# Kernel optimization log

Measured on AMD Instinct MI355X. Metric: run time of the kernel, lower is better.

The kernel has to match this reference:

```python
import jax, jax.numpy as jnp
import numpy as np

TAU = 0.8
N, D = 4096, 512

def _proj(x, W, b):
    # nn.Linear then ELU (torch Linear: x @ W.T + b)
    return jax.nn.elu(x @ W.T + b)

def setup_inputs() -> dict:
    key = jax.random.key(0)
    k1, k2, k3, k4, k5 = jax.random.split(key, 5)
    v1 = jax.random.normal(k1, (N, D), dtype=jnp.float32)
    v2 = jax.random.normal(k2, (N, D), dtype=jnp.float32)
    pos = jax.random.uniform(k3, (N, N), dtype=jnp.float32)
    neg = jax.random.uniform(k4, (N, N), dtype=jnp.float32)
    W = jax.random.normal(k5, (D, D), dtype=jnp.float32) * (1.414 / np.sqrt(D))
    b = jnp.zeros((D,), dtype=jnp.float32)
    return {"v1_embs": v1, "v2_embs": v2, "pos": pos, "neg": neg, "W_proj": W, "b_proj": b}

def reference(v1_embs, v2_embs, pos, neg, W_proj, b_proj):
    z1 = _proj(v1_embs, W_proj, b_proj)
    z2 = _proj(v2_embs, W_proj, b_proj)
    # cosine-similarity style: dot / (|z1||z2|) / tau, then exp
    n1 = jnp.linalg.norm(z1, axis=-1, keepdims=True)  # [N,1]
    n2 = jnp.linalg.norm(z2, axis=-1, keepdims=True)  # [N,1]
    dots = z1 @ z2.T                                   # [N,N]
    sim = jnp.exp(dots / (n1 * n2.T) / TAU)
    sim_pos = sim * pos
    sim_neg = sim * neg
    ratio = sim_pos.sum() / (sim_pos + sim_neg).sum()
    return -jnp.log(ratio)
```

## Files before the change

### kernel.cpp

```cpp
#include <hip/hip_runtime.h>
#include <hip/hip_bf16.h>
#include <math.h>

#define NROWS 4096
#define DDIM  512
#define INV_TAU 1.25f
#define SROW 132

typedef __attribute__((ext_vector_type(8))) short short8;
typedef __attribute__((ext_vector_type(4))) float f32x4;

__device__ inline void gload_lds16(const void* g, void* l) {
  __builtin_amdgcn_global_load_lds(
      (const __attribute__((address_space(1))) void*)g,
      (__attribute__((address_space(3))) void*)l, 16, 0, 0);
}

__device__ inline unsigned short f2bf(float f) {
  __hip_bfloat16 h = __float2bfloat16(f);
  return __builtin_bit_cast(unsigned short, h);
}
__device__ inline float bf2f(unsigned short u) {
  return __bfloat162float(__builtin_bit_cast(__hip_bfloat16, u));
}

__global__ void convert_kernel(const float* __restrict__ v1,
                               const float* __restrict__ v2,
                               const float* __restrict__ W,
                               unsigned short* __restrict__ v1b,
                               unsigned short* __restrict__ v2b,
                               unsigned short* __restrict__ Wb,
                               float* __restrict__ nsq1,
                               float* __restrict__ nsq2) {
  int idx = blockIdx.x * blockDim.x + threadIdx.x;
  if (idx < NROWS) { nsq1[idx] = 0.f; nsq2[idx] = 0.f; }
  const int TOTV = (NROWS * DDIM) / 4;
  const int TOTW = (DDIM * DDIM) / 4;
  const int total = 2 * TOTV + TOTW;
  const int stride = gridDim.x * blockDim.x;
  for (int i = idx; i < total; i += stride) {
    const float4* src; unsigned short* dst; int j;
    if (i < TOTV)            { src = (const float4*)v1; dst = v1b; j = i; }
    else if (i < 2 * TOTV)   { src = (const float4*)v2; dst = v2b; j = i - TOTV; }
    else                     { src = (const float4*)W;  dst = Wb;  j = i - 2 * TOTV; }
    float4 x = src[j];
    ushort4 o;
    o.x = f2bf(x.x); o.y = f2bf(x.y); o.z = f2bf(x.z); o.w = f2bf(x.w);
    *(ushort4*)&dst[j * 4] = o;
  }
}

#define MM_CORE(Ag, Bg)                                                        \
  {                                                                            \
    for (int kt = 0; kt < DDIM; kt += 32) {                                    \
      _Pragma("unroll")                                                        \
      for (int i = 0; i < 2; ++i) {                                            \
        int off = i * 4096 + tid * 16;            \
        int row = off >> 6;                       \
        int kb  = off & 63;                                                    \
        gload_lds16((const char*)((Ag) + row * DDIM + kt) + kb,                \
                    (char*)As + i * 4096 + wid * 1024);                        \
        gload_lds16((const char*)((Bg) + row * DDIM + kt) + kb,                \
                    (char*)Bs + i * 4096 + wid * 1024);                        \
      }                                                                        \
      asm volatile("s_waitcnt vmcnt(0)" ::: "memory");                         \
      __syncthreads();                                                         \
      short8 av[4], bv[4];                                                     \
      _Pragma("unroll")                                                        \
      for (int m = 0; m < 4; ++m)                                              \
        av[m] = *(const short8*)&As[(wm * 64 + m * 16 + l15) * 32 + l4 * 8];   \
      _Pragma("unroll")                                                        \
      for (int n = 0; n < 4; ++n)                                              \
        bv[n] = *(const short8*)&Bs[(wn * 64 + n * 16 + l15) * 32 + l4 * 8];   \
      _Pragma("unroll")                                                        \
      for (int m = 0; m < 4; ++m)                                              \
        _Pragma("unroll")                                                      \
        for (int n = 0; n < 4; ++n)                                            \
          acc[m][n] = __builtin_amdgcn_mfma_f32_16x16x32_bf16(                 \
              av[m], bv[n], acc[m][n], 0, 0, 0);                               \
      __syncthreads();                                                         \
    }                                                                          \
  }

__global__ __launch_bounds__(256) void proj_kernel(
    const unsigned short* __restrict__ v1b, const unsigned short* __restrict__ v2b,
    const unsigned short* __restrict__ Wb,  const float* __restrict__ bias,
    unsigned short* __restrict__ z1b, unsigned short* __restrict__ z2b,
    float* __restrict__ nsq1, float* __restrict__ nsq2) {
  __shared__ __align__(16) unsigned short As[128 * 32];
  __shared__ __align__(16) unsigned short Bs[128 * 32];
  const int tid = threadIdx.x;
  const int wid = tid >> 6, lane = tid & 63;
  const int wm = wid >> 1, wn = wid & 1;
  const int l15 = lane & 15, l4 = lane >> 4;

  const int zsel = blockIdx.z;
  const unsigned short* Ag = (zsel ? v2b : v1b) + (size_t)blockIdx.y * 128 * DDIM;
  const unsigned short* Bg = Wb + (size_t)blockIdx.x * 128 * DDIM;
  unsigned short* Z = (zsel ? z2b : z1b);
  float* nsq = (zsel ? nsq2 : nsq1);

  f32x4 acc[4][4];
#pragma unroll
  for (int m = 0; m < 4; ++m)
#pragma unroll
    for (int n = 0; n < 4; ++n) acc[m][n] = (f32x4){0.f, 0.f, 0.f, 0.f};

  MM_CORE(Ag, Bg);

  const int rowBase = blockIdx.y * 128 + wm * 64;
  const int colBase = blockIdx.x * 128 + wn * 64;
  float bcol[4];
#pragma unroll
  for (int n = 0; n < 4; ++n) bcol[n] = bias[colBase + n * 16 + l15];
#pragma unroll
  for (int m = 0; m < 4; ++m) {
#pragma unroll
    for (int reg = 0; reg < 4; ++reg) {
      int gRow = rowBase + m * 16 + l4 * 4 + reg;
      float rs = 0.f;
#pragma unroll
      for (int n = 0; n < 4; ++n) {
        int gCol = colBase + n * 16 + l15;
        float y = acc[m][n][reg] + bcol[n];
        float zv = (y > 0.f) ? y : expm1f(y);
        unsigned short zb = f2bf(zv);
        Z[(size_t)gRow * DDIM + gCol] = zb;
        float zf = bf2f(zb);
        rs += zf * zf;
      }
      rs += __shfl_xor(rs, 1, 64);
      rs += __shfl_xor(rs, 2, 64);
      rs += __shfl_xor(rs, 4, 64);
      rs += __shfl_xor(rs, 8, 64);
      if (l15 == 0) atomicAdd(&nsq[gRow], rs);
    }
  }
}

__global__ __launch_bounds__(256) void dots_kernel(
    const unsigned short* __restrict__ z1b, const unsigned short* __restrict__ z2b,
    const float* __restrict__ nsq1, const float* __restrict__ nsq2,
    const float* __restrict__ pos, const float* __restrict__ neg,
    double* __restrict__ partials) {
  __shared__ __align__(16) char smem[32 * SROW * 4];
  unsigned short* As = (unsigned short*)smem;
  unsigned short* Bs = (unsigned short*)(smem + 8192);
  float* sCh = (float*)smem;

  const int tid = threadIdx.x;
  const int wid = tid >> 6, lane = tid & 63;
  const int wm = wid >> 1, wn = wid & 1;
  const int l15 = lane & 15, l4 = lane >> 4;

  const unsigned short* Ag = z1b + (size_t)blockIdx.y * 128 * DDIM;
  const unsigned short* Bg = z2b + (size_t)blockIdx.x * 128 * DDIM;

  f32x4 acc[4][4];
#pragma unroll
  for (int m = 0; m < 4; ++m)
#pragma unroll
    for (int n = 0; n < 4; ++n) acc[m][n] = (f32x4){0.f, 0.f, 0.f, 0.f};

  MM_CORE(Ag, Bg);

  const int blockRow = blockIdx.y * 128;
  const int blockCol = blockIdx.x * 128;
  const int rowBase = blockRow + wm * 64;
  const int colBase = blockCol + wn * 64;

  float rs2[4];
#pragma unroll
  for (int n = 0; n < 4; ++n) rs2[n] = rsqrtf(nsq2[colBase + n * 16 + l15]);

  const int lr = tid >> 3;
  const int lcBase = (tid & 7) * 16;
  const int gRowRbase = blockRow + (lr >> 4) * 64 + (lr & 15);
  const int lrW = wm * 16 + l4 * 4;
  const int lcW = wn * 64 + l15;

  float sumP = 0.f, sumT = 0.f;
#pragma unroll
  for (int m = 0; m < 4; ++m) {
    const float* pr = pos + (size_t)(gRowRbase + m * 16) * NROWS + blockCol + lcBase;
    const float* gr = neg + (size_t)(gRowRbase + m * 16) * NROWS + blockCol + lcBase;
    float4 pv[4], gv[4];
#pragma unroll
    for (int i = 0; i < 4; ++i) {
      pv[i] = *(const float4*)(pr + 4 * i);
      gv[i] = *(const float4*)(gr + 4 * i);
    }
#pragma unroll
    for (int reg = 0; reg < 4; ++reg) {
      float rs1 = rsqrtf(nsq1[rowBase + m * 16 + l4 * 4 + reg]);
#pragma unroll
      for (int n = 0; n < 4; ++n) {
        float s = __expf(acc[m][n][reg] * (rs1 * rs2[n]) * INV_TAU);
        sCh[(lrW + reg) * SROW + lcW + n * 16] = s;
      }
    }
    __syncthreads();
#pragma unroll
    for (int i = 0; i < 4; ++i) {
      float4 s4 = *(const float4*)&sCh[lr * SROW + lcBase + 4 * i];
      sumP += s4.x * pv[i].x + s4.y * pv[i].y + s4.z * pv[i].z + s4.w * pv[i].w;
      sumT += s4.x * (pv[i].x + gv[i].x) + s4.y * (pv[i].y + gv[i].y) +
              s4.z * (pv[i].z + gv[i].z) + s4.w * (pv[i].w + gv[i].w);
    }
    __syncthreads();
  }

#pragma unroll
  for (int sft = 1; sft < 64; sft <<= 1) {
    sumP += __shfl_xor(sumP, sft, 64);
    sumT += __shfl_xor(sumT, sft, 64);
  }
  __shared__ float redP[4], redT[4];
  if (lane == 0) { redP[wid] = sumP; redT[wid] = sumT; }
  __syncthreads();
  if (tid == 0) {
    double tp = (double)redP[0] + redP[1] + redP[2] + redP[3];
    double tt = (double)redT[0] + redT[1] + redT[2] + redT[3];
    int bid = blockIdx.y * gridDim.x + blockIdx.x;
    partials[2 * bid]     = tp;
    partials[2 * bid + 1] = tt;
  }
}

__global__ void finalize_kernel(const double* __restrict__ partials,
                                float* __restrict__ out) {
  __shared__ double sp[256], st[256];
  int t = threadIdx.x;
  double a = 0.0, b = 0.0;
  for (int i = t; i < 1024; i += 256) {
    a += partials[2 * i];
    b += partials[2 * i + 1];
  }
  sp[t] = a; st[t] = b;
  __syncthreads();
  for (int s = 128; s > 0; s >>= 1) {
    if (t < s) { sp[t] += sp[t + s]; st[t] += st[t + s]; }
    __syncthreads();
  }
  if (t == 0) out[0] = (float)(log(st[0]) - log(sp[0]));
}

extern "C" void kernel_launch(void* const* d_in, const int* in_sizes, int n_in,
                              void* d_out, int out_size, void* d_ws, size_t ws_size,
                              hipStream_t stream) {
  (void)in_sizes; (void)n_in; (void)out_size; (void)ws_size;
  const float* v1   = (const float*)d_in[0];
  const float* v2   = (const float*)d_in[1];
  const float* pos  = (const float*)d_in[2];
  const float* neg  = (const float*)d_in[3];
  const float* W    = (const float*)d_in[4];
  const float* bias = (const float*)d_in[5];

  char* ws = (char*)d_ws;
  unsigned short* z1b = (unsigned short*)(ws + 0);
  unsigned short* z2b = (unsigned short*)(ws + 4194304);
  unsigned short* v1b = (unsigned short*)(ws + 8388608);
  unsigned short* v2b = (unsigned short*)(ws + 12582912);
  unsigned short* Wb  = (unsigned short*)(ws + 16777216);
  float* nsq1         = (float*)(ws + 17301504);
  float* nsq2         = (float*)(ws + 17317888);
  double* partials    = (double*)(ws + 17334272);
  float* out = (float*)d_out;

  hipLaunchKernelGGL(convert_kernel, dim3(1024), dim3(256), 0, stream,
                     v1, v2, W, v1b, v2b, Wb, nsq1, nsq2);
  hipLaunchKernelGGL(proj_kernel, dim3(DDIM / 128, NROWS / 128, 2), dim3(256), 0, stream,
                     v1b, v2b, Wb, bias, z1b, z2b, nsq1, nsq2);
  hipLaunchKernelGGL(dots_kernel, dim3(NROWS / 128, NROWS / 128), dim3(256), 0, stream,
                     z1b, z2b, nsq1, nsq2, pos, neg, partials);
  hipLaunchKernelGGL(finalize_kernel, dim3(1), dim3(256), 0, stream,
                     partials, out);
}
```

Baseline: 78.86 us.

## Double-buffer dots GEMM LDS loads, swizzle block order, prefetch pos/neg tiles

The dots kernel now stages the next K-tile into a second LDS buffer while computing MFMAs on the current one, removing the serialized load-wait-compute pattern. The grid becomes 1D with an XCD-style swizzle that maps consecutive blocks to different tile groups, aiming to improve L2 reuse of the z1/z2 rows. The epilogue prefetches the next pos/neg row chunk while computing exp values and hoists the rsqrt norm loads. In exchange LDS use doubles to 32KB and register pressure rises, which may reduce occupancy.

```diff
diff --git a/kernel.cpp b/kernel.cpp
--- a/kernel.cpp
+++ b/kernel.cpp
@@ -50,38 +50,6 @@
   }
 }
 
-#define MM_CORE(Ag, Bg)                                                        \
-  {                                                                            \
-    for (int kt = 0; kt < DDIM; kt += 32) {                                    \
-      _Pragma("unroll")                                                        \
-      for (int i = 0; i < 2; ++i) {                                            \
-        int off = i * 4096 + tid * 16;            \
-        int row = off >> 6;                       \
-        int kb  = off & 63;                                                    \
-        gload_lds16((const char*)((Ag) + row * DDIM + kt) + kb,                \
-                    (char*)As + i * 4096 + wid * 1024);                        \
-        gload_lds16((const char*)((Bg) + row * DDIM + kt) + kb,                \
-                    (char*)Bs + i * 4096 + wid * 1024);                        \
-      }                                                                        \
-      asm volatile("s_waitcnt vmcnt(0)" ::: "memory");                         \
-      __syncthreads();                                                         \
-      short8 av[4], bv[4];                                                     \
-      _Pragma("unroll")                                                        \
-      for (int m = 0; m < 4; ++m)                                              \
-        av[m] = *(const short8*)&As[(wm * 64 + m * 16 + l15) * 32 + l4 * 8];   \
-      _Pragma("unroll")                                                        \
-      for (int n = 0; n < 4; ++n)                                              \
-        bv[n] = *(const short8*)&Bs[(wn * 64 + n * 16 + l15) * 32 + l4 * 8];   \
-      _Pragma("unroll")                                                        \
-      for (int m = 0; m < 4; ++m)                                              \
-        _Pragma("unroll")                                                      \
-        for (int n = 0; n < 4; ++n)                                            \
-          acc[m][n] = __builtin_amdgcn_mfma_f32_16x16x32_bf16(                 \
-              av[m], bv[n], acc[m][n], 0, 0, 0);                               \
-      __syncthreads();                                                         \
-    }                                                                          \
-  }
-
 __global__ __launch_bounds__(256) void proj_kernel(
     const unsigned short* __restrict__ v1b, const unsigned short* __restrict__ v2b,
     const unsigned short* __restrict__ Wb,  const float* __restrict__ bias,
@@ -106,7 +74,34 @@
 #pragma unroll
     for (int n = 0; n < 4; ++n) acc[m][n] = (f32x4){0.f, 0.f, 0.f, 0.f};
 
-  MM_CORE(Ag, Bg);
+  for (int kt = 0; kt < DDIM; kt += 32) {
+#pragma unroll
+    for (int i = 0; i < 2; ++i) {
+      int off = i * 4096 + tid * 16;
+      int row = off >> 6;
+      int kb  = off & 63;
+      gload_lds16((const char*)(Ag + row * DDIM + kt) + kb,
+                  (char*)As + i * 4096 + wid * 1024);
+      gload_lds16((const char*)(Bg + row * DDIM + kt) + kb,
+                  (char*)Bs + i * 4096 + wid * 1024);
+    }
+    asm volatile("s_waitcnt vmcnt(0)" ::: "memory");
+    __syncthreads();
+    short8 av[4], bv[4];
+#pragma unroll
+    for (int m = 0; m < 4; ++m)
+      av[m] = *(const short8*)&As[(wm * 64 + m * 16 + l15) * 32 + l4 * 8];
+#pragma unroll
+    for (int n = 0; n < 4; ++n)
+      bv[n] = *(const short8*)&Bs[(wn * 64 + n * 16 + l15) * 32 + l4 * 8];
+#pragma unroll
+    for (int m = 0; m < 4; ++m)
+#pragma unroll
+      for (int n = 0; n < 4; ++n)
+        acc[m][n] = __builtin_amdgcn_mfma_f32_16x16x32_bf16(
+            av[m], bv[n], acc[m][n], 0, 0, 0);
+    __syncthreads();
+  }
 
   const int rowBase = blockIdx.y * 128 + wm * 64;
   const int colBase = blockIdx.x * 128 + wn * 64;
@@ -143,9 +138,7 @@
     const float* __restrict__ nsq1, const float* __restrict__ nsq2,
     const float* __restrict__ pos, const float* __restrict__ neg,
     double* __restrict__ partials) {
-  __shared__ __align__(16) char smem[32 * SROW * 4];
-  unsigned short* As = (unsigned short*)smem;
-  unsigned short* Bs = (unsigned short*)(smem + 8192);
+  __shared__ __align__(16) char smem[2][16384];
   float* sCh = (float*)smem;
 
   const int tid = threadIdx.x;
@@ -153,8 +146,12 @@
   const int wm = wid >> 1, wn = wid & 1;
   const int l15 = lane & 15, l4 = lane >> 4;
 
-  const unsigned short* Ag = z1b + (size_t)blockIdx.y * 128 * DDIM;
-  const unsigned short* Bg = z2b + (size_t)blockIdx.x * 128 * DDIM;
+  const int bid = blockIdx.x;
+  const int swz = (bid & 7) * 128 + (bid >> 3);
+  const int by = swz >> 5, bx = swz & 31;
+
+  const unsigned short* Ag = z1b + (size_t)by * 128 * DDIM;
+  const unsigned short* Bg = z2b + (size_t)bx * 128 * DDIM;
 
   f32x4 acc[4][4];
 #pragma unroll
@@ -162,16 +159,52 @@
 #pragma unroll
     for (int n = 0; n < 4; ++n) acc[m][n] = (f32x4){0.f, 0.f, 0.f, 0.f};
 
-  MM_CORE(Ag, Bg);
-
-  const int blockRow = blockIdx.y * 128;
-  const int blockCol = blockIdx.x * 128;
+#define STAGE(buf, kt)                                                         \
+  {                                                                            \
+    _Pragma("unroll")                                                          \
+    for (int i = 0; i < 2; ++i) {                                              \
+      int off = i * 4096 + tid * 16;                                           \
+      int row = off >> 6;                                                      \
+      int kb  = off & 63;                                                      \
+      gload_lds16((const char*)(Ag + row * DDIM + (kt)) + kb,                  \
+                  smem[buf] + i * 4096 + wid * 1024);                          \
+      gload_lds16((const char*)(Bg + row * DDIM + (kt)) + kb,                  \
+                  smem[buf] + 8192 + i * 4096 + wid * 1024);                   \
+    }                                                                          \
+  }
+
+  STAGE(0, 0);
+  asm volatile("s_waitcnt vmcnt(0)" ::: "memory");
+  __syncthreads();
+
+#pragma unroll
+  for (int t = 0; t < 16; ++t) {
+    const int cur = t & 1;
+    if (t < 15) STAGE(cur ^ 1, (t + 1) * 32);
+    const unsigned short* As = (const unsigned short*)smem[cur];
+    const unsigned short* Bs = (const unsigned short*)(smem[cur] + 8192);
+    short8 av[4], bv[4];
+#pragma unroll
+    for (int m = 0; m < 4; ++m)
+      av[m] = *(const short8*)&As[(wm * 64 + m * 16 + l15) * 32 + l4 * 8];
+#pragma unroll
+    for (int n = 0; n < 4; ++n)
+      bv[n] = *(const short8*)&Bs[(wn * 64 + n * 16 + l15) * 32 + l4 * 8];
+#pragma unroll
+    for (int m = 0; m < 4; ++m)
+#pragma unroll
+      for (int n = 0; n < 4; ++n)
+        acc[m][n] = __builtin_amdgcn_mfma_f32_16x16x32_bf16(
+            av[m], bv[n], acc[m][n], 0, 0, 0);
+    asm volatile("s_waitcnt vmcnt(0)" ::: "memory");
+    __syncthreads();
+  }
+#undef STAGE
+
+  const int blockRow = by * 128;
+  const int blockCol = bx * 128;
   const int rowBase = blockRow + wm * 64;
   const int colBase = blockCol + wn * 64;
-
-  float rs2[4];
-#pragma unroll
-  for (int n = 0; n < 4; ++n) rs2[n] = rsqrtf(nsq2[colBase + n * 16 + l15]);
 
   const int lr = tid >> 3;
   const int lcBase = (tid & 7) * 16;
@@ -179,33 +212,54 @@
   const int lrW = wm * 16 + l4 * 4;
   const int lcW = wn * 64 + l15;
 
+  float4 pv[2][4], gv[2][4];
+  {
+    const float* pr = pos + (size_t)gRowRbase * NROWS + blockCol + lcBase;
+    const float* gr = neg + (size_t)gRowRbase * NROWS + blockCol + lcBase;
+#pragma unroll
+    for (int i = 0; i < 4; ++i) {
+      pv[0][i] = *(const float4*)(pr + 4 * i);
+      gv[0][i] = *(const float4*)(gr + 4 * i);
+    }
+  }
+
+  float rs2[4], rs1[4][4];
+#pragma unroll
+  for (int n = 0; n < 4; ++n) rs2[n] = rsqrtf(nsq2[colBase + n * 16 + l15]);
+#pragma unroll
+  for (int m = 0; m < 4; ++m)
+#pragma unroll
+    for (int reg = 0; reg < 4; ++reg)
+      rs1[m][reg] = rsqrtf(nsq1[rowBase + m * 16 + l4 * 4 + reg]);
+
   float sumP = 0.f, sumT = 0.f;
 #pragma unroll
   for (int m = 0; m < 4; ++m) {
-    const float* pr = pos + (size_t)(gRowRbase + m * 16) * NROWS + blockCol + lcBase;
-    const float* gr = neg + (size_t)(gRowRbase + m * 16) * NROWS + blockCol + lcBase;
-    float4 pv[4], gv[4];
-#pragma unroll
-    for (int i = 0; i < 4; ++i) {
-      pv[i] = *(const float4*)(pr + 4 * i);
-      gv[i] = *(const float4*)(gr + 4 * i);
-    }
+    const int c = m & 1, o = c ^ 1;
 #pragma unroll
     for (int reg = 0; reg < 4; ++reg) {
-      float rs1 = rsqrtf(nsq1[rowBase + m * 16 + l4 * 4 + reg]);
 #pragma unroll
       for (int n = 0; n < 4; ++n) {
-        float s = __expf(acc[m][n][reg] * (rs1 * rs2[n]) * INV_TAU);
+        float s = __expf(acc[m][n][reg] * (rs1[m][reg] * rs2[n]) * INV_TAU);
         sCh[(lrW + reg) * SROW + lcW + n * 16] = s;
       }
     }
+    if (m < 3) {
+      const float* pr = pos + (size_t)(gRowRbase + (m + 1) * 16) * NROWS + blockCol + lcBase;
+      const float* gr = neg + (size_t)(gRowRbase + (m + 1) * 16) * NROWS + blockCol + lcBase;
+#pragma unroll
+      for (int i = 0; i < 4; ++i) {
+        pv[o][i] = *(const float4*)(pr + 4 * i);
+        gv[o][i] = *(const float4*)(gr + 4 * i);
+      }
+    }
     __syncthreads();
 #pragma unroll
     for (int i = 0; i < 4; ++i) {
       float4 s4 = *(const float4*)&sCh[lr * SROW + lcBase + 4 * i];
-      sumP += s4.x * pv[i].x + s4.y * pv[i].y + s4.z * pv[i].z + s4.w * pv[i].w;
-      sumT += s4.x * (pv[i].x + gv[i].x) + s4.y * (pv[i].y + gv[i].y) +
-              s4.z * (pv[i].z + gv[i].z) + s4.w * (pv[i].w + gv[i].w);
+      sumP += s4.x * pv[c][i].x + s4.y * pv[c][i].y + s4.z * pv[c][i].z + s4.w * pv[c][i].w;
+      sumT += s4.x * (pv[c][i].x + gv[c][i].x) + s4.y * (pv[c][i].y + gv[c][i].y) +
+              s4.z * (pv[c][i].z + gv[c][i].z) + s4.w * (pv[c][i].w + gv[c][i].w);
     }
     __syncthreads();
   }
@@ -221,7 +275,6 @@
   if (tid == 0) {
     double tp = (double)redP[0] + redP[1] + redP[2] + redP[3];
     double tt = (double)redT[0] + redT[1] + redT[2] + redT[3];
-    int bid = blockIdx.y * gridDim.x + blockIdx.x;
     partials[2 * bid]     = tp;
     partials[2 * bid + 1] = tt;
   }
@@ -271,7 +324,7 @@
                      v1, v2, W, v1b, v2b, Wb, nsq1, nsq2);
   hipLaunchKernelGGL(proj_kernel, dim3(DDIM / 128, NROWS / 128, 2), dim3(256), 0, stream,
                      v1b, v2b, Wb, bias, z1b, z2b, nsq1, nsq2);
-  hipLaunchKernelGGL(dots_kernel, dim3(NROWS / 128, NROWS / 128), dim3(256), 0, stream,
+  hipLaunchKernelGGL(dots_kernel, dim3(1024), dim3(256), 0, stream,
                      z1b, z2b, nsq1, nsq2, pos, neg, partials);
   hipLaunchKernelGGL(finalize_kernel, dim3(1), dim3(256), 0, stream,
                      partials, out);
```

After: 85.71 us. +8.7%, slower.
